# Kernel tuning notes

Measured on AMD Instinct MI355X. Metric: run time of the kernel, lower is better.

The kernel has to match this reference:

```python
import jax, jax.numpy as jnp
import numpy as np


def _pairwise_dist(pred, gt):
    # pred: [B, N, 3], gt: [B, M, 3] -> Euclidean distances [B, N, M]
    p2 = jnp.sum(pred * pred, axis=-1)  # [B, N]
    g2 = jnp.sum(gt * gt, axis=-1)      # [B, M]
    cross = jnp.einsum('bnd,bmd->bnm', pred, gt)  # [B, N, M]
    d2 = p2[:, :, None] + g2[:, None, :] - 2.0 * cross
    return jnp.sqrt(jnp.maximum(d2, 1e-12))


def setup_inputs() -> dict:
    key = jax.random.key(0)
    k1, k2 = jax.random.split(key)
    pred = jax.random.normal(k1, (32, 4096, 3), dtype=jnp.float32)
    gt = jax.random.normal(k2, (32, 4096, 3), dtype=jnp.float32)
    return {"pred": pred, "gt": gt}


def reference(pred, gt):
    dist = _pairwise_dist(pred, gt)              # [B, N, M]
    chamfer1 = jnp.mean(jnp.min(dist, axis=1))   # min over pred points (dim=1)
    chamfer2 = jnp.mean(jnp.min(dist, axis=2))   # min over gt points (dim=2)
    return chamfer1 + chamfer2
```

## Files before the change

kernel.cpp:

```cpp
#include <hip/hip_runtime.h>
#include <math.h>


typedef short short8 __attribute__((ext_vector_type(8)));
typedef float f32x16 __attribute__((ext_vector_type(16)));
typedef unsigned int uint;

#define NPTS  4096
#define TPBM  512
#define TPBP  256
#define NPANEL 8
#define GRID_MAIN (2 * 32 * NPANEL)
#define NBT   128
#define CHT   32
#define NCH   4
#define ONEB ((short)0x3F80)

__device__ __forceinline__ unsigned short bf16h(float f) {
    uint u = __float_as_uint(f);
    uint r = u + 0x7FFFu + ((u >> 16) & 1u);
    return (unsigned short)(r >> 16);
}
__device__ __forceinline__ float bf16f(unsigned short h) {
    return __uint_as_float(((uint)h) << 16);
}
struct Split2 { unsigned short h, m; };
__device__ __forceinline__ Split2 split2(float x) {
    Split2 s;
    s.h = bf16h(x);
    s.m = bf16h(x - bf16f(s.h));
    return s;
}

__global__ __launch_bounds__(TPBP) void chamfer_prep(
    const float* __restrict__ pred, const float* __restrict__ gt,
    short8* __restrict__ Bfrag)
{
    const int gid  = blockIdx.x * TPBP + threadIdx.x;
    const int lane = gid & 63;
    const int ent  = gid >> 6;
    const int side = ent >> 12;
    const int b    = (ent >> 7) & 31;
    const int tile = ent & 127;
    const int c31  = lane & 31, half = lane >> 5;

    const float* src = side ? gt : pred;
    const float* p = src + ((size_t)(b * NPTS + tile * 32 + c31)) * 3;
    float x = p[0], y = p[1], z = p[2];
    Split2 X = split2(x), Y = split2(y), Z = split2(z);
    Split2 T2 = split2(fmaf(x, x, fmaf(y, y, z * z)));

    short8 f;
    if (half == 0) {
        f[0]=(short)X.h; f[1]=(short)Y.h; f[2]=(short)Z.h;
        f[3]=(short)X.m; f[4]=(short)Y.m; f[5]=(short)Z.m;
        f[6]=(short)X.h; f[7]=(short)Y.h;
    } else {
        f[0]=(short)Z.h; f[1]=(short)X.m; f[2]=(short)Y.m; f[3]=(short)Z.m;
        f[4]=ONEB;       f[5]=ONEB;       f[6]=(short)T2.h; f[7]=(short)T2.m;
    }
    Bfrag[gid] = f;
}

__global__ __launch_bounds__(TPBM, 4) void chamfer_mfma(
    const float* __restrict__ pred,
    const float* __restrict__ gt,
    float* __restrict__ wsgt,
    const short8* __restrict__ Bfrag)
{
    const int bx    = blockIdx.x;
    const int dir   = bx >> 8;
    const int rem   = bx & 255;
    const int b     = rem >> 3;
    const int panel = rem & 7;
    const int tid   = threadIdx.x;
    const int lane  = tid & 63, wid = tid >> 6;
    const int c31   = lane & 31, half = lane >> 5;

    __shared__ short8 sB[CHT * 64];
    __shared__ float  sw[8];

    const float* qsrc = (dir ? pred : gt) + (size_t)b * NPTS * 3;
    const size_t bfb  = ((size_t)dir * 32 + b) * (NBT * 64);

    short8 afr[2];
    float gm[2][16];
#pragma unroll
    for (int fr = 0; fr < 2; ++fr) {
        const int row = panel * 512 + wid * 64 + fr * 32 + c31;
        const float* ap = qsrc + (size_t)row * 3;
        float x = ap[0], y = ap[1], z = ap[2];
        Split2 X = split2(-2.0f*x), Y = split2(-2.0f*y), Z = split2(-2.0f*z);
        Split2 Q2 = split2(fmaf(x, x, fmaf(y, y, z * z)));
        short8 a;
        if (half == 0) {
            a[0]=(short)X.h; a[1]=(short)Y.h; a[2]=(short)Z.h;
            a[3]=(short)X.h; a[4]=(short)Y.h; a[5]=(short)Z.h;
            a[6]=(short)X.m; a[7]=(short)Y.m;
        } else {
            a[0]=(short)Z.m; a[1]=(short)X.m; a[2]=(short)Y.m; a[3]=(short)Z.m;
            a[4]=(short)Q2.h; a[5]=(short)Q2.m; a[6]=ONEB; a[7]=ONEB;
        }
        afr[fr] = a;
#pragma unroll
        for (int r = 0; r < 16; ++r) gm[fr][r] = 1e30f;
    }

    const f32x16 zero = {0.f,0.f,0.f,0.f,0.f,0.f,0.f,0.f,
                         0.f,0.f,0.f,0.f,0.f,0.f,0.f,0.f};

    short8 pf[4];
#pragma unroll
    for (int ps = 0; ps < 4; ++ps) {
        const int u = ps * TPBM + tid;
        pf[ps] = Bfrag[bfb + (size_t)u];
    }

    for (int ch = 0; ch < NCH; ++ch) {
        __syncthreads();
#pragma unroll
        for (int ps = 0; ps < 4; ++ps) sB[ps * TPBM + tid] = pf[ps];
        __syncthreads();

        const int chn = (ch + 1 < NCH) ? ch + 1 : ch;
#pragma unroll
        for (int ps = 0; ps < 4; ++ps) {
            const int u = ps * TPBM + tid;
            pf[ps] = Bfrag[bfb + (size_t)(chn * (CHT * 64) + u)];
        }

#pragma unroll 4
        for (int t = 0; t < CHT; ++t) {
            short8 bfr = sB[t * 64 + lane];
            f32x16 a0 = __builtin_amdgcn_mfma_f32_32x32x16_bf16(
                afr[0], bfr, zero, 0, 0, 0);
            f32x16 a1 = __builtin_amdgcn_mfma_f32_32x32x16_bf16(
                afr[1], bfr, zero, 0, 0, 0);
#pragma unroll
            for (int r = 0; r < 16; ++r) {
                gm[0][r] = fminf(gm[0][r], a0[r]);
                gm[1][r] = fminf(gm[1][r], a1[r]);
            }
        }
    }

#pragma unroll
    for (int off = 1; off < 32; off <<= 1)
#pragma unroll
        for (int fr = 0; fr < 2; ++fr)
#pragma unroll
            for (int r = 0; r < 16; ++r)
                gm[fr][r] = fminf(gm[fr][r], __shfl_xor(gm[fr][r], off, 64));

    float s = 0.0f;
    if (c31 == 0) {
#pragma unroll
        for (int fr = 0; fr < 2; ++fr)
#pragma unroll
            for (int r = 0; r < 16; ++r)
                s += sqrtf(fmaxf(gm[fr][r], 1e-12f));
    }
    s += __shfl_xor(s, 32, 64);
    if (lane == 0) sw[wid] = s;
    __syncthreads();
    if (tid == 0)
        wsgt[bx] = sw[0]+sw[1]+sw[2]+sw[3]+sw[4]+sw[5]+sw[6]+sw[7];
}

__global__ __launch_bounds__(TPBP) void chamfer_finish(
    const float* __restrict__ wsgt, float* __restrict__ out)
{
    __shared__ float swv[TPBP / 64];
    const int tid = threadIdx.x;

    float s = 0.0f;
#pragma unroll
    for (int r = 0; r < GRID_MAIN / TPBP; ++r)
        s += wsgt[tid + r * TPBP];

#pragma unroll
    for (int off = 32; off > 0; off >>= 1) s += __shfl_down(s, off, 64);
    const int wid = tid >> 6, lane = tid & 63;
    if (lane == 0) swv[wid] = s;
    __syncthreads();
    if (tid == 0)
        out[0] = (swv[0] + swv[1] + swv[2] + swv[3]) * (1.0f / 131072.0f);
}

extern "C" void kernel_launch(void* const* d_in, const int* in_sizes, int n_in,
                              void* d_out, int out_size, void* d_ws, size_t ws_size,
                              hipStream_t stream)
{
    const float* pred = (const float*)d_in[0];
    const float* gt   = (const float*)d_in[1];
    float* out        = (float*)d_out;

    float*  wsgt  = (float*)d_ws;
    short8* Bfrag = (short8*)((char*)d_ws + (1 << 20));

    chamfer_prep<<<dim3((2 * 32 * NBT * 64) / TPBP), dim3(TPBP), 0, stream>>>(
        pred, gt, Bfrag);
    chamfer_mfma<<<dim3(GRID_MAIN), dim3(TPBM), 0, stream>>>(
        pred, gt, wsgt, Bfrag);
    chamfer_finish<<<dim3(1), dim3(TPBP), 0, stream>>>(wsgt, out);
}
```

Baseline: 105.8 us.

## Halve MFMA block size, double panels, shrink LDS chunks, pair B tiles per step

Each block now runs 256 threads over 256 query rows instead of 512, so the grid has twice as many blocks, and each LDS chunk holds 8 gt tiles instead of 32 across 16 chunks. The inner loop now loads two B fragments at a time and folds the results of two MFMAs with a three-operand min chain. The aims are more blocks for better CU balance and fewer dependent min operations. In exchange there are four times as many barriers per block, and B data is re-read from global memory by twice as many blocks.

```diff
diff --git a/kernel.cpp b/kernel.cpp
--- a/kernel.cpp
+++ b/kernel.cpp
@@ -7,13 +7,13 @@
 typedef unsigned int uint;
 
 #define NPTS  4096
-#define TPBM  512
+#define TPBM  256
 #define TPBP  256
-#define NPANEL 8
+#define NPANEL 16
 #define GRID_MAIN (2 * 32 * NPANEL)
 #define NBT   128
-#define CHT   32
-#define NCH   4
+#define CHT   8
+#define NCH   16
 #define ONEB ((short)0x3F80)
 
 __device__ __forceinline__ unsigned short bf16h(float f) {
@@ -69,16 +69,16 @@
     const short8* __restrict__ Bfrag)
 {
     const int bx    = blockIdx.x;
-    const int dir   = bx >> 8;
-    const int rem   = bx & 255;
-    const int b     = rem >> 3;
-    const int panel = rem & 7;
+    const int dir   = bx >> 9;
+    const int rem   = bx & 511;
+    const int b     = rem >> 4;
+    const int panel = rem & 15;
     const int tid   = threadIdx.x;
     const int lane  = tid & 63, wid = tid >> 6;
     const int c31   = lane & 31, half = lane >> 5;
 
     __shared__ short8 sB[CHT * 64];
-    __shared__ float  sw[8];
+    __shared__ float  sw[4];
 
     const float* qsrc = (dir ? pred : gt) + (size_t)b * NPTS * 3;
     const size_t bfb  = ((size_t)dir * 32 + b) * (NBT * 64);
@@ -87,7 +87,7 @@
     float gm[2][16];
 #pragma unroll
     for (int fr = 0; fr < 2; ++fr) {
-        const int row = panel * 512 + wid * 64 + fr * 32 + c31;
+        const int row = panel * 256 + wid * 64 + fr * 32 + c31;
         const float* ap = qsrc + (size_t)row * 3;
         float x = ap[0], y = ap[1], z = ap[2];
         Split2 X = split2(-2.0f*x), Y = split2(-2.0f*y), Z = split2(-2.0f*z);
@@ -109,38 +109,40 @@
     const f32x16 zero = {0.f,0.f,0.f,0.f,0.f,0.f,0.f,0.f,
                          0.f,0.f,0.f,0.f,0.f,0.f,0.f,0.f};
 
-    short8 pf[4];
-#pragma unroll
-    for (int ps = 0; ps < 4; ++ps) {
-        const int u = ps * TPBM + tid;
-        pf[ps] = Bfrag[bfb + (size_t)u];
-    }
+    short8 pf[2];
+#pragma unroll
+    for (int ps = 0; ps < 2; ++ps)
+        pf[ps] = Bfrag[bfb + (size_t)(ps * TPBM + tid)];
 
     for (int ch = 0; ch < NCH; ++ch) {
         __syncthreads();
 #pragma unroll
-        for (int ps = 0; ps < 4; ++ps) sB[ps * TPBM + tid] = pf[ps];
+        for (int ps = 0; ps < 2; ++ps) sB[ps * TPBM + tid] = pf[ps];
         __syncthreads();
 
         const int chn = (ch + 1 < NCH) ? ch + 1 : ch;
 #pragma unroll
-        for (int ps = 0; ps < 4; ++ps) {
-            const int u = ps * TPBM + tid;
-            pf[ps] = Bfrag[bfb + (size_t)(chn * (CHT * 64) + u)];
-        }
-
-#pragma unroll 4
-        for (int t = 0; t < CHT; ++t) {
-            short8 bfr = sB[t * 64 + lane];
-            f32x16 a0 = __builtin_amdgcn_mfma_f32_32x32x16_bf16(
-                afr[0], bfr, zero, 0, 0, 0);
-            f32x16 a1 = __builtin_amdgcn_mfma_f32_32x32x16_bf16(
-                afr[1], bfr, zero, 0, 0, 0);
-#pragma unroll
-            for (int r = 0; r < 16; ++r) {
-                gm[0][r] = fminf(gm[0][r], a0[r]);
-                gm[1][r] = fminf(gm[1][r], a1[r]);
-            }
+        for (int ps = 0; ps < 2; ++ps)
+            pf[ps] = Bfrag[bfb + (size_t)(chn * (CHT * 64) + ps * TPBM + tid)];
+
+#pragma unroll
+        for (int tp = 0; tp < CHT / 2; ++tp) {
+            short8 b0 = sB[(2 * tp) * 64 + lane];
+            short8 b1 = sB[(2 * tp + 1) * 64 + lane];
+            f32x16 a00 = __builtin_amdgcn_mfma_f32_32x32x16_bf16(
+                afr[0], b0, zero, 0, 0, 0);
+            f32x16 a01 = __builtin_amdgcn_mfma_f32_32x32x16_bf16(
+                afr[0], b1, zero, 0, 0, 0);
+#pragma unroll
+            for (int r = 0; r < 16; ++r)
+                gm[0][r] = fminf(fminf(a00[r], a01[r]), gm[0][r]);
+            f32x16 a10 = __builtin_amdgcn_mfma_f32_32x32x16_bf16(
+                afr[1], b0, zero, 0, 0, 0);
+            f32x16 a11 = __builtin_amdgcn_mfma_f32_32x32x16_bf16(
+                afr[1], b1, zero, 0, 0, 0);
+#pragma unroll
+            for (int r = 0; r < 16; ++r)
+                gm[1][r] = fminf(fminf(a10[r], a11[r]), gm[1][r]);
         }
     }
 
@@ -164,7 +166,7 @@
     if (lane == 0) sw[wid] = s;
     __syncthreads();
     if (tid == 0)
-        wsgt[bx] = sw[0]+sw[1]+sw[2]+sw[3]+sw[4]+sw[5]+sw[6]+sw[7];
+        wsgt[bx] = sw[0] + sw[1] + sw[2] + sw[3];
 }
 
 __global__ __launch_bounds__(TPBP) void chamfer_finish(
```

After: 104.3 us. About the same (-1.5%).
